# Performance work log

Measured on AMD Instinct MI355X. Metric: run time of the kernel, lower is better.

The kernel has to match this reference:

```python
import jax, jax.numpy as jnp
import numpy as np

N_QUBITS = 10
Q_DEPTH = 6


def _apply_1q(state, gate, wire):
    """Apply a 2x2 gate (or batched [B,2,2] gates) to `wire` of state [B,2,...,2]."""
    s = jnp.moveaxis(state, wire + 1, -1)
    if gate.ndim == 2:
        s = s @ gate.T  # new_j = sum_i G[j,i] * old_i
    else:
        s = jnp.einsum('b...i,bji->b...j', s, gate)
    return jnp.moveaxis(s, -1, wire + 1)


def _apply_cnot(state, ctrl, tgt):
    s = jnp.moveaxis(state, (ctrl + 1, tgt + 1), (-2, -1))
    s = jnp.stack([s[..., 0, :], s[..., 1, ::-1]], axis=-2)  # flip target where ctrl=1
    return jnp.moveaxis(s, (-2, -1), (ctrl + 1, tgt + 1))


def _ry(theta):
    """RY(theta) = [[cos(t/2), -sin(t/2)], [sin(t/2), cos(t/2)]]; theta scalar or [B]."""
    c, s = jnp.cos(theta / 2.0), jnp.sin(theta / 2.0)
    return jnp.stack([jnp.stack([c, -s], -1), jnp.stack([s, c], -1)], -2)


def _vqc(angles, q_weights):
    """angles: [B, n_qubits] per-sample RY angles; q_weights: [q_depth, n_qubits].
    Returns <PauliZ_w> for every wire: [B, n_qubits]. All gates are real -> float32 state."""
    B, n = angles.shape
    q_depth = q_weights.shape[0]
    # H-layer on |0...0> gives the uniform superposition: all amplitudes 2^{-n/2}
    state = jnp.full((B,) + (2,) * n, 2.0 ** (-n / 2.0), dtype=angles.dtype)
    # RY layer with per-sample input angles
    for w in range(n):
        state = _apply_1q(state, _ry(angles[:, w]), w)
    # q_depth x (brick-wall CNOT entangler + trainable RY layer)
    for k in range(q_depth):
        for i in range(0, n - 1, 2):
            state = _apply_cnot(state, i, i + 1)
        for i in range(1, n - 1, 2):
            state = _apply_cnot(state, i, i + 1)
        for w in range(n):
            state = _apply_1q(state, _ry(q_weights[k, w]), w)
    # expval(PauliZ(w)) = P(wire w = 0) - P(wire w = 1)
    probs = state * state  # real statevector
    exps = []
    for w in range(n):
        p = jnp.moveaxis(probs, w + 1, 1).reshape(B, 2, -1).sum(-1)
        exps.append(p[:, 0] - p[:, 1])
    return jnp.stack(exps, -1)


def setup_inputs() -> dict:
    key = jax.random.key(0)
    ks = jax.random.split(key, 6)
    B, D_IN, OUT = 8192, 512, 64
    x = jax.random.normal(ks[0], (B, D_IN), dtype=jnp.float32)
    W1 = jax.random.normal(ks[1], (D_IN, N_QUBITS), dtype=jnp.float32) * (1.0 / np.sqrt(D_IN))
    b1 = jnp.zeros((N_QUBITS,), dtype=jnp.float32)
    # keras 'uniform' initializer: U(-0.05, 0.05)
    q_weights = jax.random.uniform(ks[2], (Q_DEPTH, N_QUBITS), dtype=jnp.float32,
                                   minval=-0.05, maxval=0.05)
    W2 = jax.random.normal(ks[3], (N_QUBITS, OUT), dtype=jnp.float32) * (1.0 / np.sqrt(N_QUBITS))
    b2 = jnp.zeros((OUT,), dtype=jnp.float32)
    return {"x": x, "W1": W1, "b1": b1, "q_weights": q_weights, "W2": W2, "b2": b2}


def reference(x, W1, b1, q_weights, W2, b2):
    # Dense(n_qubits, tanh) then scale to angles in (-pi/2, pi/2)
    angles = jnp.tanh(x @ W1 + b1) * (jnp.pi / 2.0)  # [B, n_qubits]
    q_out = _vqc(angles, q_weights)                   # [B, n_qubits]
    return q_out @ W2 + b2                            # [B, output_dim]
```

## Files before the change

### kernel.cpp

```cpp
#include <hip/hip_runtime.h>

#define NQ 10
#define QD 6
#define DIN 512
#define DOUT 64

typedef float v2f __attribute__((ext_vector_type(2)));

__device__ __forceinline__ v2f sp(float s) { v2f r; r.x = s; r.y = s; return r; }
__device__ __forceinline__ v2f mk(float a, float b) { v2f r; r.x = a; r.y = b; return r; }

__device__ __forceinline__ v2f pk_fma(v2f a, v2f b, v2f c) {
    v2f d; asm("v_pk_fma_f32 %0, %1, %2, %3" : "=v"(d) : "v"(a), "v"(b), "v"(c)); return d;
}
__device__ __forceinline__ v2f pk_mul(v2f a, v2f b) {
    v2f d; asm("v_pk_mul_f32 %0, %1, %2" : "=v"(d) : "v"(a), "v"(b)); return d;
}
__device__ __forceinline__ v2f pk_add(v2f a, v2f b) {
    v2f d; asm("v_pk_add_f32 %0, %1, %2" : "=v"(d) : "v"(a), "v"(b)); return d;
}

template <int CTRL>
__device__ __forceinline__ float dppf(float v) {
    return __int_as_float(__builtin_amdgcn_mov_dpp(__float_as_int(v), CTRL, 0xF, 0xF, true));
}
template <int M>
__device__ __forceinline__ float sx(float v) {
    if constexpr (M == 1)       return dppf<0xB1>(v);
    else if constexpr (M == 2)  return dppf<0x4E>(v);
    else if constexpr (M == 4)  return dppf<0x1B>(dppf<0x141>(v));
    else if constexpr (M == 8)  return dppf<0x128>(v);
    else                        return __int_as_float(__builtin_amdgcn_ds_swizzle(__float_as_int(v), 0x401F));
}
__device__ __forceinline__ float sx32(float v, int xaddr) {
    return __int_as_float(__builtin_amdgcn_ds_bpermute(xaddr, __float_as_int(v)));
}
template <int M>
__device__ __forceinline__ v2f sx2(v2f v) { return mk(sx<M>(v.x), sx<M>(v.y)); }
__device__ __forceinline__ float red64(float v, int xaddr) {
    v += dppf<0x128>(v);
    v += dppf<0x124>(v);
    v += dppf<0x122>(v);
    v += dppf<0x121>(v);
    v += __int_as_float(__builtin_amdgcn_ds_swizzle(__float_as_int(v), 0x401F));
    v += sx32(v, xaddr);
    return v;
}

__global__ __launch_bounds__(256, 6) void dqc_main(
    const float* __restrict__ x,
    const float* __restrict__ W1,
    const float* __restrict__ b1,
    const float* __restrict__ qw,
    const float* __restrict__ W2,
    const float* __restrict__ b2,
    float* __restrict__ out,
    const int B)
{
    __shared__ __align__(16) float csl[QD * 24];

    const int tid = threadIdx.x;
    if (tid < QD * NQ) {
        const int layer = tid / NQ, wire = tid - layer * NQ;
        float s, c;
        sincosf(qw[tid] * 0.5f, &s, &c);
        const int pos = layer * 24 + (wire & 1) * 12 + (wire >> 1) * 2;
        csl[pos] = c; csl[pos + 1] = s;
    }

    const int lane = tid & 63;
    const int b = blockIdx.x * 4 + (tid >> 6);
    const int bb = (b < B) ? b : (B - 1);
    const int xaddr = ((tid ^ 32) & 63) << 2;

    float xr[8];
    {
        const float4* xp = (const float4*)(x + (size_t)bb * DIN + lane * 8);
        const float4 v0 = xp[0], v1 = xp[1];
        xr[0]=v0.x; xr[1]=v0.y; xr[2]=v0.z; xr[3]=v0.w;
        xr[4]=v1.x; xr[5]=v1.y; xr[6]=v1.z; xr[7]=v1.w;
    }
    float dot[NQ];
    #pragma unroll
    for (int w = 0; w < NQ; ++w) dot[w] = 0.f;
    {
        const float4* wp = (const float4*)(W1 + (size_t)lane * 8 * NQ);
        #pragma unroll
        for (int j = 0; j < 4; ++j) {
            const float4 f0 = wp[5*j], f1 = wp[5*j+1], f2 = wp[5*j+2],
                         f3 = wp[5*j+3], f4 = wp[5*j+4];
            const float xa = xr[2*j], xb = xr[2*j+1];
            dot[0]=fmaf(xa,f0.x,dot[0]); dot[1]=fmaf(xa,f0.y,dot[1]);
            dot[2]=fmaf(xa,f0.z,dot[2]); dot[3]=fmaf(xa,f0.w,dot[3]);
            dot[4]=fmaf(xa,f1.x,dot[4]); dot[5]=fmaf(xa,f1.y,dot[5]);
            dot[6]=fmaf(xa,f1.z,dot[6]); dot[7]=fmaf(xa,f1.w,dot[7]);
            dot[8]=fmaf(xa,f2.x,dot[8]); dot[9]=fmaf(xa,f2.y,dot[9]);
            dot[0]=fmaf(xb,f2.z,dot[0]); dot[1]=fmaf(xb,f2.w,dot[1]);
            dot[2]=fmaf(xb,f3.x,dot[2]); dot[3]=fmaf(xb,f3.y,dot[3]);
            dot[4]=fmaf(xb,f3.z,dot[4]); dot[5]=fmaf(xb,f3.w,dot[5]);
            dot[6]=fmaf(xb,f4.x,dot[6]); dot[7]=fmaf(xb,f4.y,dot[7]);
            dot[8]=fmaf(xb,f4.z,dot[8]); dot[9]=fmaf(xb,f4.w,dot[9]);
        }
    }
    #pragma unroll
    for (int w = 0; w < NQ; ++w) dot[w] = red64(dot[w], xaddr);

    float u0[NQ], u1[NQ];
    #pragma unroll
    for (int w = 0; w < NQ; ++w) {
        const float th2 = tanhf(dot[w] + b1[w]) * 0.78539816339744830962f;
        float s, c;
        sincosf(th2, &s, &c);
        const float isq2 = 0.70710678118654752440f;
        u0[w] = (c - s) * isq2;
        u1[w] = (c + s) * isq2;
    }

    v2f A[8];
    {
        float lf = ((lane & 32) ? u1[0] : u0[0]);
        lf *= ((((lane >> 4) ^ (lane >> 5)) & 1) ? u1[1] : u0[1]);
        lf *= ((lane & 8) ? u1[2] : u0[2]);
        lf *= ((((lane >> 2) ^ (lane >> 3)) & 1) ? u1[3] : u0[3]);
        lf *= ((lane & 2) ? u1[4] : u0[4]);
        lf *= (((lane ^ (lane >> 1)) & 1) ? u1[5] : u0[5]);
        #pragma unroll
        for (int m = 0; m < 8; ++m) {
            float f = ((m & 4) ? u1[6] : u0[6]);
            f *= ((((m >> 1) ^ (m >> 2)) & 1) ? u1[7] : u0[7]);
            f *= ((m & 1) ? u1[8] : u0[8]);
            f *= lf;
            A[m] = (m & 1) ? mk(f * u1[9], f * u0[9]) : mk(f * u0[9], f * u1[9]);
        }
    }

    __syncthreads();

    #pragma unroll 1
    for (int k = 0; k < QD; ++k) {
        const float* ce = csl + k * 24;
        const bool fuse = (k != QD - 1);

        const float4 ea = *(const float4*)(ce);
        const float4 eb = *(const float4*)(ce + 4);
        const float2 ec = *(const float2*)(ce + 8);
        const float C0=ea.x, S0=ea.y, C2=ea.z, S2=ea.w;
        const float C4=eb.x, S4=eb.y, C6=eb.z, S6=eb.w;
        const float C8=ec.x, S8=ec.y;

        {
            const float g = (lane & 32) ? S0 : -S0;
            const v2f alv = sp(C0), bev = sp(g);
            #pragma unroll
            for (int m = 0; m < 8; ++m) {
                const v2f p = mk(sx32(A[m].x, xaddr), sx32(A[m].y, xaddr));
                A[m] = pk_fma(alv, A[m], pk_mul(bev, p));
            }
        }
        {
            const float g = (lane & 8) ? S2 : -S2;
            const bool cb = (lane & 16) != 0;
            const v2f alv = sp(cb ? g : C2), bev = sp(cb ? C2 : g);
            #pragma unroll
            for (int m = 0; m < 8; ++m) {
                const v2f p = sx2<8>(A[m]);
                A[m] = pk_fma(alv, A[m], pk_mul(bev, p));
            }
        }
        {
            const float g = (lane & 2) ? S4 : -S4;
            const bool cb = (lane & 4) != 0;
            const v2f alv = sp(cb ? g : C4), bev = sp(cb ? C4 : g);
            #pragma unroll
            for (int m = 0; m < 8; ++m) {
                const v2f p = sx2<2>(A[m]);
                A[m] = pk_fma(alv, A[m], pk_mul(bev, p));
            }
        }
        {
            const bool cb = (lane & 1) != 0;
            const v2f a_lo = sp(cb ? -S6 : C6), b_lo = sp(cb ? C6 : -S6);
            const v2f a_hi = sp(cb ?  S6 : C6), b_hi = sp(cb ? C6 :  S6);
            #pragma unroll
            for (int m = 0; m < 4; ++m) {
                const v2f lo = A[m], hi = A[m + 4];
                A[m]     = pk_fma(a_lo, lo, pk_mul(b_lo, hi));
                A[m + 4] = pk_fma(a_hi, hi, pk_mul(b_hi, lo));
            }
        }
        {
            const v2f c8 = sp(C8), s8 = sp(S8), ns8 = sp(-S8);
            #pragma unroll
            for (int m = 0; m < 8; m += 2) {
                const v2f lo = A[m], hi = A[m + 1];
                if (m & 2) {
                    A[m]     = pk_fma(ns8, lo, pk_mul(c8, hi));
                    A[m + 1] = pk_fma(s8,  hi, pk_mul(c8, lo));
                } else {
                    A[m]     = pk_fma(c8, lo, pk_mul(ns8, hi));
                    A[m + 1] = pk_fma(c8, hi, pk_mul(s8,  lo));
                }
            }
        }

        const float4 oa = *(const float4*)(ce + 12);
        const float4 ob = *(const float4*)(ce + 16);
        const float2 oc = *(const float2*)(ce + 20);
        const float C1=oa.x, S1=oa.y, C3=oa.z, S3=oa.w;
        const float C5=ob.x, S5=ob.y, C7=ob.z, S7=ob.w;
        const float C9=oc.x, S9=oc.y;

        {
            const float g = (lane & 16) ? S1 : -S1;
            const bool cb = fuse && ((lane & 32) != 0);
            const v2f alv = sp(cb ? -g : C1), bev = sp(cb ? C1 : g);
            #pragma unroll
            for (int m = 0; m < 8; ++m) {
                const v2f p = sx2<16>(A[m]);
                A[m] = pk_fma(alv, A[m], pk_mul(bev, p));
            }
        }
        {
            const float g = (lane & 4) ? S3 : -S3;
            const bool cb = fuse && ((lane & 8) != 0);
            const v2f alv = sp(cb ? -g : C3), bev = sp(cb ? C3 : g);
            #pragma unroll
            for (int m = 0; m < 8; ++m) {
                const v2f p = sx2<4>(A[m]);
                A[m] = pk_fma(alv, A[m], pk_mul(bev, p));
            }
        }
        {
            const float g = (lane & 1) ? S5 : -S5;
            const bool cb = fuse && ((lane & 2) != 0);
            const v2f alv = sp(cb ? -g : C5), bev = sp(cb ? C5 : g);
            #pragma unroll
            for (int m = 0; m < 8; ++m) {
                const v2f p = sx2<1>(A[m]);
                A[m] = pk_fma(alv, A[m], pk_mul(bev, p));
            }
        }
        {
            const v2f c7 = sp(C7), s7 = sp(S7), ns7 = sp(-S7);
            const v2f a_lo4 = fuse ? s7 : c7,  b_lo4 = fuse ? c7 : ns7;
            const v2f a_hi4 = fuse ? ns7 : c7, b_hi4 = fuse ? c7 : s7;
            #pragma unroll
            for (int m = 0; m < 2; ++m) {
                {   const v2f lo = A[m], hi = A[m + 2];
                    A[m]     = pk_fma(c7, lo, pk_mul(ns7, hi));
                    A[m + 2] = pk_fma(c7, hi, pk_mul(s7,  lo)); }
                {   const v2f lo = A[m + 4], hi = A[m + 6];
                    A[m + 4] = pk_fma(a_lo4, lo, pk_mul(b_lo4, hi));
                    A[m + 6] = pk_fma(a_hi4, hi, pk_mul(b_hi4, lo)); }
            }
        }
        {
            const float nS9 = -S9;
            const float axx = fuse ? S9 : C9,  axy = fuse ? C9 : nS9;
            const float ayy = fuse ? nS9 : C9, ayx = fuse ? C9 : S9;
            #pragma unroll
            for (int m = 0; m < 8; ++m) {
                const float ax = A[m].x, ay = A[m].y;
                if (m & 1) {
                    A[m].x = fmaf(axx, ax, axy * ay);
                    A[m].y = fmaf(ayy, ay, ayx * ax);
                } else {
                    A[m].x = fmaf(C9, ax, nS9 * ay);
                    A[m].y = fmaf(C9, ay, S9  * ax);
                }
            }
        }
    }

    v2f P[8];
    #pragma unroll
    for (int m = 0; m < 8; ++m) P[m] = pk_mul(A[m], A[m]);
    const v2f s01 = pk_add(P[0], P[1]), s23 = pk_add(P[2], P[3]);
    const v2f s45 = pk_add(P[4], P[5]), s67 = pk_add(P[6], P[7]);
    const v2f q8v = pk_add(pk_add(P[1], P[3]), pk_add(P[5], P[7]));
    const v2f q6v = pk_add(s45, s67);
    const v2f q7v = pk_add(s23, s67);
    const v2f tot2 = pk_add(pk_add(s01, s23), q6v);
    const float tot = tot2.x + tot2.y;

    float e[NQ];
    e[0] = (lane & 32) ? -tot : tot;
    e[1] = (lane & 16) ? -tot : tot;
    e[2] = (lane & 8)  ? -tot : tot;
    e[3] = (lane & 4)  ? -tot : tot;
    e[4] = (lane & 2)  ? -tot : tot;
    e[5] = (lane & 1)  ? -tot : tot;
    e[6] = fmaf(-2.f, q6v.x + q6v.y, tot);
    e[7] = fmaf(-2.f, q7v.x + q7v.y, tot);
    e[8] = fmaf(-2.f, q8v.x + q8v.y, tot);
    e[9] = fmaf(-2.f, tot2.y, tot);
    #pragma unroll
    for (int w = 0; w < NQ; ++w) e[w] = red64(e[w], xaddr);

    if (b < B) {
        float o = b2[lane];
        #pragma unroll
        for (int w = 0; w < NQ; ++w) o = fmaf(e[w], W2[w * DOUT + lane], o);
        out[(size_t)b * DOUT + lane] = o;
    }
}

extern "C" void kernel_launch(void* const* d_in, const int* in_sizes, int n_in,
                              void* d_out, int out_size, void* d_ws, size_t ws_size,
                              hipStream_t stream) {
    const float* x  = (const float*)d_in[0];
    const float* W1 = (const float*)d_in[1];
    const float* b1 = (const float*)d_in[2];
    const float* qw = (const float*)d_in[3];
    const float* W2 = (const float*)d_in[4];
    const float* b2 = (const float*)d_in[5];
    float* out = (float*)d_out;

    const int B = in_sizes[0] / DIN;
    const int blocks = (B + 3) / 4;
    dqc_main<<<blocks, 256, 0, stream>>>(x, W1, b1, qw, W2, b2, out, B);
}
```

Baseline: 106.6 us.

## Replace packed-FMA gate kernel with scalar DPP-fused FMAC and fast transcendentals

Drops the packed v2f state layout in favour of 16 scalar amplitudes per lane. Lane-crossing gates now use v_fmac_f32_dpp, which folds the cross-lane move into the FMA, with sched_barriers to control ordering. tanh, sin and cos switch to fast intrinsics, and the initial RY stage is written as a single cos/sin of a shifted angle. Occupancy hint drops from 6 to 4, and the fast math loses some accuracy.

```diff
diff --git a/kernel.cpp b/kernel.cpp
--- a/kernel.cpp
+++ b/kernel.cpp
@@ -5,20 +5,40 @@
 #define DIN 512
 #define DOUT 64
 
-typedef float v2f __attribute__((ext_vector_type(2)));
-
-__device__ __forceinline__ v2f sp(float s) { v2f r; r.x = s; r.y = s; return r; }
-__device__ __forceinline__ v2f mk(float a, float b) { v2f r; r.x = a; r.y = b; return r; }
-
-__device__ __forceinline__ v2f pk_fma(v2f a, v2f b, v2f c) {
-    v2f d; asm("v_pk_fma_f32 %0, %1, %2, %3" : "=v"(d) : "v"(a), "v"(b), "v"(c)); return d;
-}
-__device__ __forceinline__ v2f pk_mul(v2f a, v2f b) {
-    v2f d; asm("v_pk_mul_f32 %0, %1, %2" : "=v"(d) : "v"(a), "v"(b)); return d;
-}
-__device__ __forceinline__ v2f pk_add(v2f a, v2f b) {
-    v2f d; asm("v_pk_add_f32 %0, %1, %2" : "=v"(d) : "v"(a), "v"(b)); return d;
-}
+#define FMAC_DPP(t, a, b, CTRL) \
+    asm("v_fmac_f32_dpp %0, %1, %2 " CTRL " row_mask:0xf bank_mask:0xf" \
+        : "+v"(t) : "v"(a), "v"(b))
+#define SB() __builtin_amdgcn_sched_barrier(0)
+
+#define LANE_GATE_DPP(CTRL, ALV, BEV)                                     \
+    {                                                                     \
+        float t[16];                                                      \
+        _Pragma("unroll")                                                 \
+        for (int r = 0; r < 16; ++r) t[r] = (ALV) * A[r];                 \
+        SB();                                                             \
+        _Pragma("unroll")                                                 \
+        for (int r = 0; r < 16; ++r) FMAC_DPP(t[r], A[r], (BEV), CTRL);   \
+        SB();                                                             \
+        _Pragma("unroll")                                                 \
+        for (int r = 0; r < 16; ++r) A[r] = t[r];                         \
+    }
+
+#define LANE_GATE_X4(ALV, BEV)                                            \
+    {                                                                     \
+        float p[16], t[16];                                               \
+        _Pragma("unroll")                                                 \
+        for (int r = 0; r < 16; ++r) p[r] = dppf<0x141>(A[r]);            \
+        SB();                                                             \
+        _Pragma("unroll")                                                 \
+        for (int r = 0; r < 16; ++r) t[r] = (ALV) * A[r];                 \
+        SB();                                                             \
+        _Pragma("unroll")                                                 \
+        for (int r = 0; r < 16; ++r)                                      \
+            FMAC_DPP(t[r], p[r], (BEV), "quad_perm:[3,2,1,0]");           \
+        SB();                                                             \
+        _Pragma("unroll")                                                 \
+        for (int r = 0; r < 16; ++r) A[r] = t[r];                         \
+    }
 
 template <int CTRL>
 __device__ __forceinline__ float dppf(float v) {
@@ -26,17 +46,12 @@
 }
 template <int M>
 __device__ __forceinline__ float sx(float v) {
-    if constexpr (M == 1)       return dppf<0xB1>(v);
-    else if constexpr (M == 2)  return dppf<0x4E>(v);
-    else if constexpr (M == 4)  return dppf<0x1B>(dppf<0x141>(v));
-    else if constexpr (M == 8)  return dppf<0x128>(v);
-    else                        return __int_as_float(__builtin_amdgcn_ds_swizzle(__float_as_int(v), 0x401F));
+    if constexpr (M == 16)
+        return __int_as_float(__builtin_amdgcn_ds_swizzle(__float_as_int(v), 0x401F));
 }
 __device__ __forceinline__ float sx32(float v, int xaddr) {
     return __int_as_float(__builtin_amdgcn_ds_bpermute(xaddr, __float_as_int(v)));
 }
-template <int M>
-__device__ __forceinline__ v2f sx2(v2f v) { return mk(sx<M>(v.x), sx<M>(v.y)); }
 __device__ __forceinline__ float red64(float v, int xaddr) {
     v += dppf<0x128>(v);
     v += dppf<0x124>(v);
@@ -47,7 +62,12 @@
     return v;
 }
 
-__global__ __launch_bounds__(256, 6) void dqc_main(
+__device__ __forceinline__ float tanh_fast(float x) {
+    const float e = __expf(2.0f * x);
+    return 1.0f - __fdividef(2.0f, e + 1.0f);
+}
+
+__global__ __launch_bounds__(256, 4) void dqc_main(
     const float* __restrict__ x,
     const float* __restrict__ W1,
     const float* __restrict__ b1,
@@ -62,10 +82,9 @@
     const int tid = threadIdx.x;
     if (tid < QD * NQ) {
         const int layer = tid / NQ, wire = tid - layer * NQ;
-        float s, c;
-        sincosf(qw[tid] * 0.5f, &s, &c);
+        const float h = qw[tid] * 0.5f;
         const int pos = layer * 24 + (wire & 1) * 12 + (wire >> 1) * 2;
-        csl[pos] = c; csl[pos + 1] = s;
+        csl[pos] = __cosf(h); csl[pos + 1] = __sinf(h);
     }
 
     const int lane = tid & 63;
@@ -108,15 +127,13 @@
     float u0[NQ], u1[NQ];
     #pragma unroll
     for (int w = 0; w < NQ; ++w) {
-        const float th2 = tanhf(dot[w] + b1[w]) * 0.78539816339744830962f;
-        float s, c;
-        sincosf(th2, &s, &c);
-        const float isq2 = 0.70710678118654752440f;
-        u0[w] = (c - s) * isq2;
-        u1[w] = (c + s) * isq2;
-    }
-
-    v2f A[8];
+        const float phi = fmaf(tanh_fast(dot[w] + b1[w]),
+                               0.78539816339744830962f, 0.78539816339744830962f);
+        u0[w] = __cosf(phi);
+        u1[w] = __sinf(phi);
+    }
+
+    float A[16];
     {
         float lf = ((lane & 32) ? u1[0] : u0[0]);
         lf *= ((((lane >> 4) ^ (lane >> 5)) & 1) ? u1[1] : u0[1]);
@@ -125,12 +142,12 @@
         lf *= ((lane & 2) ? u1[4] : u0[4]);
         lf *= (((lane ^ (lane >> 1)) & 1) ? u1[5] : u0[5]);
         #pragma unroll
-        for (int m = 0; m < 8; ++m) {
-            float f = ((m & 4) ? u1[6] : u0[6]);
-            f *= ((((m >> 1) ^ (m >> 2)) & 1) ? u1[7] : u0[7]);
-            f *= ((m & 1) ? u1[8] : u0[8]);
-            f *= lf;
-            A[m] = (m & 1) ? mk(f * u1[9], f * u0[9]) : mk(f * u0[9], f * u1[9]);
+        for (int r = 0; r < 16; ++r) {
+            float f = ((r & 8) ? u1[6] : u0[6]);
+            f *= ((((r >> 2) ^ (r >> 3)) & 1) ? u1[7] : u0[7]);
+            f *= ((r & 2) ? u1[8] : u0[8]);
+            f *= ((((r >> 1) ^ r) & 1) ? u1[9] : u0[9]);
+            A[r] = f * lf;
         }
     }
 
@@ -144,61 +161,52 @@
         const float4 ea = *(const float4*)(ce);
         const float4 eb = *(const float4*)(ce + 4);
         const float2 ec = *(const float2*)(ce + 8);
-        const float C0=ea.x, S0=ea.y, C2=ea.z, S2=ea.w;
-        const float C4=eb.x, S4=eb.y, C6=eb.z, S6=eb.w;
-        const float C8=ec.x, S8=ec.y;
+        const float C0=ea.x,S0=ea.y, C2=ea.z,S2=ea.w;
+        const float C4=eb.x,S4=eb.y, C6=eb.z,S6=eb.w;
+        const float C8=ec.x,S8=ec.y;
 
         {
             const float g = (lane & 32) ? S0 : -S0;
-            const v2f alv = sp(C0), bev = sp(g);
-            #pragma unroll
-            for (int m = 0; m < 8; ++m) {
-                const v2f p = mk(sx32(A[m].x, xaddr), sx32(A[m].y, xaddr));
-                A[m] = pk_fma(alv, A[m], pk_mul(bev, p));
-            }
+            float p[16];
+            #pragma unroll
+            for (int r = 0; r < 16; ++r) p[r] = sx32(A[r], xaddr);
+            #pragma unroll
+            for (int r = 0; r < 16; ++r) A[r] = fmaf(C0, A[r], g * p[r]);
         }
         {
             const float g = (lane & 8) ? S2 : -S2;
             const bool cb = (lane & 16) != 0;
-            const v2f alv = sp(cb ? g : C2), bev = sp(cb ? C2 : g);
-            #pragma unroll
-            for (int m = 0; m < 8; ++m) {
-                const v2f p = sx2<8>(A[m]);
-                A[m] = pk_fma(alv, A[m], pk_mul(bev, p));
-            }
+            const float alv = cb ? g : C2, bev = cb ? C2 : g;
+            LANE_GATE_DPP("row_ror:8", alv, bev);
         }
         {
             const float g = (lane & 2) ? S4 : -S4;
             const bool cb = (lane & 4) != 0;
-            const v2f alv = sp(cb ? g : C4), bev = sp(cb ? C4 : g);
-            #pragma unroll
-            for (int m = 0; m < 8; ++m) {
-                const v2f p = sx2<2>(A[m]);
-                A[m] = pk_fma(alv, A[m], pk_mul(bev, p));
+            const float alv = cb ? g : C4, bev = cb ? C4 : g;
+            LANE_GATE_DPP("quad_perm:[2,3,0,1]", alv, bev);
+        }
+        {
+            const bool cb = (lane & 1) != 0;
+            const float a_lo = cb ? -S6 : C6, b_lo = cb ? C6 : -S6;
+            const float a_hi = cb ?  S6 : C6, b_hi = cb ? C6 :  S6;
+            #pragma unroll
+            for (int r = 0; r < 8; ++r) {
+                const float lo = A[r], hi = A[r + 8];
+                A[r]     = fmaf(a_lo, lo, b_lo * hi);
+                A[r + 8] = fmaf(a_hi, hi, b_hi * lo);
             }
         }
         {
-            const bool cb = (lane & 1) != 0;
-            const v2f a_lo = sp(cb ? -S6 : C6), b_lo = sp(cb ? C6 : -S6);
-            const v2f a_hi = sp(cb ?  S6 : C6), b_hi = sp(cb ? C6 :  S6);
-            #pragma unroll
-            for (int m = 0; m < 4; ++m) {
-                const v2f lo = A[m], hi = A[m + 4];
-                A[m]     = pk_fma(a_lo, lo, pk_mul(b_lo, hi));
-                A[m + 4] = pk_fma(a_hi, hi, pk_mul(b_hi, lo));
-            }
-        }
-        {
-            const v2f c8 = sp(C8), s8 = sp(S8), ns8 = sp(-S8);
-            #pragma unroll
-            for (int m = 0; m < 8; m += 2) {
-                const v2f lo = A[m], hi = A[m + 1];
-                if (m & 2) {
-                    A[m]     = pk_fma(ns8, lo, pk_mul(c8, hi));
-                    A[m + 1] = pk_fma(s8,  hi, pk_mul(c8, lo));
+            #pragma unroll
+            for (int r = 0; r < 16; ++r) {
+                if (r & 2) continue;
+                const float lo = A[r], hi = A[r + 2];
+                if (r & 4) {
+                    A[r]     = fmaf(-S8, lo, C8 * hi);
+                    A[r + 2] = fmaf( S8, hi, C8 * lo);
                 } else {
-                    A[m]     = pk_fma(c8, lo, pk_mul(ns8, hi));
-                    A[m + 1] = pk_fma(c8, hi, pk_mul(s8,  lo));
+                    A[r]     = fmaf(C8, lo, -S8 * hi);
+                    A[r + 2] = fmaf(C8, hi,  S8 * lo);
                 }
             }
         }
@@ -206,83 +214,71 @@
         const float4 oa = *(const float4*)(ce + 12);
         const float4 ob = *(const float4*)(ce + 16);
         const float2 oc = *(const float2*)(ce + 20);
-        const float C1=oa.x, S1=oa.y, C3=oa.z, S3=oa.w;
-        const float C5=ob.x, S5=ob.y, C7=ob.z, S7=ob.w;
-        const float C9=oc.x, S9=oc.y;
+        const float C1=oa.x,S1=oa.y, C3=oa.z,S3=oa.w;
+        const float C5=ob.x,S5=ob.y, C7=ob.z,S7=ob.w;
+        const float C9=oc.x,S9=oc.y;
 
         {
             const float g = (lane & 16) ? S1 : -S1;
             const bool cb = fuse && ((lane & 32) != 0);
-            const v2f alv = sp(cb ? -g : C1), bev = sp(cb ? C1 : g);
-            #pragma unroll
-            for (int m = 0; m < 8; ++m) {
-                const v2f p = sx2<16>(A[m]);
-                A[m] = pk_fma(alv, A[m], pk_mul(bev, p));
-            }
+            const float alv = cb ? -g : C1, bev = cb ? C1 : g;
+            float p[16];
+            #pragma unroll
+            for (int r = 0; r < 16; ++r) p[r] = sx<16>(A[r]);
+            #pragma unroll
+            for (int r = 0; r < 16; ++r) A[r] = fmaf(alv, A[r], bev * p[r]);
         }
         {
             const float g = (lane & 4) ? S3 : -S3;
             const bool cb = fuse && ((lane & 8) != 0);
-            const v2f alv = sp(cb ? -g : C3), bev = sp(cb ? C3 : g);
-            #pragma unroll
-            for (int m = 0; m < 8; ++m) {
-                const v2f p = sx2<4>(A[m]);
-                A[m] = pk_fma(alv, A[m], pk_mul(bev, p));
-            }
+            const float alv = cb ? -g : C3, bev = cb ? C3 : g;
+            LANE_GATE_X4(alv, bev);
         }
         {
             const float g = (lane & 1) ? S5 : -S5;
             const bool cb = fuse && ((lane & 2) != 0);
-            const v2f alv = sp(cb ? -g : C5), bev = sp(cb ? C5 : g);
-            #pragma unroll
-            for (int m = 0; m < 8; ++m) {
-                const v2f p = sx2<1>(A[m]);
-                A[m] = pk_fma(alv, A[m], pk_mul(bev, p));
-            }
-        }
-        {
-            const v2f c7 = sp(C7), s7 = sp(S7), ns7 = sp(-S7);
-            const v2f a_lo4 = fuse ? s7 : c7,  b_lo4 = fuse ? c7 : ns7;
-            const v2f a_hi4 = fuse ? ns7 : c7, b_hi4 = fuse ? c7 : s7;
-            #pragma unroll
-            for (int m = 0; m < 2; ++m) {
-                {   const v2f lo = A[m], hi = A[m + 2];
-                    A[m]     = pk_fma(c7, lo, pk_mul(ns7, hi));
-                    A[m + 2] = pk_fma(c7, hi, pk_mul(s7,  lo)); }
-                {   const v2f lo = A[m + 4], hi = A[m + 6];
-                    A[m + 4] = pk_fma(a_lo4, lo, pk_mul(b_lo4, hi));
-                    A[m + 6] = pk_fma(a_hi4, hi, pk_mul(b_hi4, lo)); }
-            }
-        }
-        {
-            const float nS9 = -S9;
-            const float axx = fuse ? S9 : C9,  axy = fuse ? C9 : nS9;
-            const float ayy = fuse ? nS9 : C9, ayx = fuse ? C9 : S9;
-            #pragma unroll
-            for (int m = 0; m < 8; ++m) {
-                const float ax = A[m].x, ay = A[m].y;
-                if (m & 1) {
-                    A[m].x = fmaf(axx, ax, axy * ay);
-                    A[m].y = fmaf(ayy, ay, ayx * ax);
+            const float alv = cb ? -g : C5, bev = cb ? C5 : g;
+            LANE_GATE_DPP("quad_perm:[1,0,3,2]", alv, bev);
+        }
+        {
+            #pragma unroll
+            for (int r = 0; r < 16; ++r) {
+                if (r & 4) continue;
+                const float lo = A[r], hi = A[r + 4];
+                if (fuse && (r & 8)) {
+                    A[r]     = fmaf( S7, lo, C7 * hi);
+                    A[r + 4] = fmaf(-S7, hi, C7 * lo);
                 } else {
-                    A[m].x = fmaf(C9, ax, nS9 * ay);
-                    A[m].y = fmaf(C9, ay, S9  * ax);
+                    A[r]     = fmaf(C7, lo, -S7 * hi);
+                    A[r + 4] = fmaf(C7, hi,  S7 * lo);
                 }
             }
         }
-    }
-
-    v2f P[8];
-    #pragma unroll
-    for (int m = 0; m < 8; ++m) P[m] = pk_mul(A[m], A[m]);
-    const v2f s01 = pk_add(P[0], P[1]), s23 = pk_add(P[2], P[3]);
-    const v2f s45 = pk_add(P[4], P[5]), s67 = pk_add(P[6], P[7]);
-    const v2f q8v = pk_add(pk_add(P[1], P[3]), pk_add(P[5], P[7]));
-    const v2f q6v = pk_add(s45, s67);
-    const v2f q7v = pk_add(s23, s67);
-    const v2f tot2 = pk_add(pk_add(s01, s23), q6v);
-    const float tot = tot2.x + tot2.y;
-
+        {
+            #pragma unroll
+            for (int r = 0; r < 16; r += 2) {
+                const float xv = A[r], yv = A[r + 1];
+                if (fuse && (r & 2)) {
+                    A[r]     = fmaf( S9, xv, C9 * yv);
+                    A[r + 1] = fmaf(-S9, yv, C9 * xv);
+                } else {
+                    A[r]     = fmaf(C9, xv, -S9 * yv);
+                    A[r + 1] = fmaf(C9, yv,  S9 * xv);
+                }
+            }
+        }
+    }
+
+    float tot = 0.f, q6 = 0.f, q7 = 0.f, q8 = 0.f, q9 = 0.f;
+    #pragma unroll
+    for (int r = 0; r < 16; ++r) {
+        const float P = A[r] * A[r];
+        tot += P;
+        if (r & 8) q6 += P;
+        if (r & 4) q7 += P;
+        if (r & 2) q8 += P;
+        if (r & 1) q9 += P;
+    }
     float e[NQ];
     e[0] = (lane & 32) ? -tot : tot;
     e[1] = (lane & 16) ? -tot : tot;
@@ -290,10 +286,10 @@
     e[3] = (lane & 4)  ? -tot : tot;
     e[4] = (lane & 2)  ? -tot : tot;
     e[5] = (lane & 1)  ? -tot : tot;
-    e[6] = fmaf(-2.f, q6v.x + q6v.y, tot);
-    e[7] = fmaf(-2.f, q7v.x + q7v.y, tot);
-    e[8] = fmaf(-2.f, q8v.x + q8v.y, tot);
-    e[9] = fmaf(-2.f, tot2.y, tot);
+    e[6] = fmaf(-2.f, q6, tot);
+    e[7] = fmaf(-2.f, q7, tot);
+    e[8] = fmaf(-2.f, q8, tot);
+    e[9] = fmaf(-2.f, q9, tot);
     #pragma unroll
     for (int w = 0; w < NQ; ++w) e[w] = red64(e[w], xaddr);
 
```

New measurement: 105.8 us. Within noise of the previous version (-0.8%).
